# Optimization experiments

Measured on AMD Instinct MI355X. Metric: run time of the kernel, lower is better.

The kernel has to match this reference:

```python
import jax, jax.numpy as jnp
import numpy as np

B, N, D, EMB, H, W = 32, 20, 512, 512, 64, 64
TEMP = 10.0
EPS_IN = 1e-5


def setup_inputs() -> dict:
    key = jax.random.key(0)
    ks = jax.random.split(key, 12)
    fvisu = jax.random.normal(ks[0], (B, D, H, W), dtype=jnp.float32)
    fword = jax.random.normal(ks[1], (B, N, D), dtype=jnp.float32)
    context_score = jax.random.uniform(ks[2], (B, N), dtype=jnp.float32)
    # contiguous valid-token mask: lengths in [3, N-1] so CLS/SEP zeroing stays in range
    lengths = jax.random.randint(ks[3], (B,), 3, N)  # < N
    word_mask = (jnp.arange(N)[None, :] < lengths[:, None]).astype(jnp.int32)
    # params (kaiming-ish scale)
    def kinit(k, shape, fan_in):
        return jax.random.normal(k, shape, dtype=jnp.float32) * np.sqrt(2.0 / fan_in)
    attn_map_w = kinit(ks[4], (EMB // 2, D), D)          # Conv1d(512,256,1)
    attn_map_b = jnp.zeros((EMB // 2,), jnp.float32)
    attn_score_w = kinit(ks[5], (EMB // 2,), EMB // 2)   # Conv1d(256,1,1)
    attn_score_b = jnp.zeros((), jnp.float32)
    gamma_w = kinit(ks[6], (2 * EMB, D), D)              # Linear(512, 1024)
    gamma_b = jnp.zeros((2 * EMB,), jnp.float32)
    conv1_w = kinit(ks[7], (EMB, D), D)                  # Conv2d(512,512,1)
    conv1_b = jnp.zeros((EMB,), jnp.float32)
    return {
        "fvisu": fvisu, "fword": fword, "context_score": context_score,
        "attn_map_w": attn_map_w, "attn_map_b": attn_map_b,
        "attn_score_w": attn_score_w, "attn_score_b": attn_score_b,
        "gamma_w": gamma_w, "gamma_b": gamma_b,
        "conv1_w": conv1_w, "conv1_b": conv1_b,
        "word_mask": word_mask,
    }


def mask_softmax(attn_score, word_mask):
    # score = softmax(attn_score * T) over words
    score = jax.nn.softmax(attn_score * TEMP, axis=1)
    n = attn_score.shape[1]
    idx = jnp.arange(n)[None, :]
    m = word_mask[:, :n].astype(jnp.float32)
    m = m * (idx != 0)                                   # zero CLS
    s = m.sum(axis=1).astype(jnp.int32)                  # sum AFTER zeroing pos 0
    m = m * (idx != s[:, None])                          # zero SEP (last valid)
    ms = score * m
    return ms / (ms.sum(axis=1, keepdims=True) + 1e-8)


def reference(fvisu, fword, context_score, attn_map_w, attn_map_b,
              attn_score_w, attn_score_b, gamma_w, gamma_b,
              conv1_w, conv1_b, word_mask):
    # fword: [B,N,D] -> fw: [B,D,N]
    fw = jnp.transpose(fword, (0, 2, 1))
    # tile_visu: mean over spatial -> [B,D,1]
    tile_visu = jnp.mean(fvisu.reshape(fvisu.shape[0], fvisu.shape[1], -1), axis=2, keepdims=True)
    # prod fusion
    context_tile = tile_visu * fw * context_score[:, None, :]           # [B,D,N]
    attn_feat = jnp.tanh(jnp.einsum('oc,bcn->bon', attn_map_w, context_tile) + attn_map_b[None, :, None])
    attn_score = jnp.einsum('c,bcn->bn', attn_score_w, attn_feat) + attn_score_b  # [B,N]
    mask_score = mask_softmax(attn_score, word_mask)
    attn_lang_my = mask_score[:, None, :] * fw                          # [B,D,N]
    attn_lang = jnp.einsum('bn,bnd->bd', mask_score, fword)             # [B,D]
    # FiLM params
    film = attn_lang @ gamma_w.T + gamma_b                              # [B,2*EMB]
    gammas = jnp.tanh(film[:, :EMB])[:, :, None, None]
    betas = jnp.tanh(film[:, EMB:])[:, :, None, None]
    # conv1 (1x1) + InstanceNorm2d (no affine)
    fmodu = jnp.einsum('oc,bchw->bohw', conv1_w, fvisu) + conv1_b[None, :, None, None]
    mu = jnp.mean(fmodu, axis=(2, 3), keepdims=True)
    var = jnp.var(fmodu, axis=(2, 3), keepdims=True)
    fmodu = (fmodu - mu) * jax.lax.rsqrt(var + EPS_IN)
    fmodu = jax.nn.relu(gammas * fmodu + betas)
    return fmodu, attn_lang_my, attn_score
```

## Files before the change

kernel.cpp:

```cpp
#include <hip/hip_runtime.h>
#include <hip/hip_bf16.h>
#include <stdint.h>

#define NW 20
#define CD 512

typedef __attribute__((ext_vector_type(8))) short bhalf8;
typedef __attribute__((ext_vector_type(4))) float floatx4;

__device__ __forceinline__ uint16_t f2bf(float f){
    __hip_bfloat16 h = __float2bfloat16(f);
    return __builtin_bit_cast(uint16_t, h);
}
__device__ __forceinline__ float bf2f(uint16_t u){
    return __uint_as_float(((uint32_t)u) << 16);
}
__device__ __forceinline__ int hsw(int r){ return ((r >> 1) ^ (r >> 2)) & 7; }

__device__ __forceinline__ void gload16(const void* g, void* l){
    __builtin_amdgcn_global_load_lds(
        (const __attribute__((address_space(1))) uint32_t*)g,
        (__attribute__((address_space(3))) uint32_t*)l, 16, 0, 0);
}

__global__ void GroundTextBlock_context_49761491091856_kernel(int* p){ if (p) *p = 0; }

__global__ __launch_bounds__(256) void kprep(const float* __restrict__ w,
                                             uint16_t* __restrict__ warr){
    int ot = blockIdx.x >> 3, ks = blockIdx.x & 7;
    uint16_t* dst = warr + (size_t)blockIdx.x * 8192;
    for (int i = threadIdx.x; i < 8192; i += 256){
        int o = i >> 6, ke = i & 63;
        float v = w[(size_t)(ot * 128 + o) * 512 + ks * 64 + ke];
        int byteoff = o * 128 + ((((ke >> 3) ^ hsw(o)) << 4)) + ((ke & 7) << 1);
        dst[byteoff >> 1] = f2bf(v);
    }
}

__global__ __launch_bounds__(256) void kgemm(const float* __restrict__ fvisu,
                                             const uint16_t* __restrict__ warr,
                                             float* __restrict__ out0){
    __shared__ __align__(16) uint8_t Ab[16384];
    __shared__ __align__(16) uint8_t Bb[16384];
    __shared__ float tsum[CD];

    int lid = (int)((blockIdx.x & 7) * 512 + (blockIdx.x >> 3));
    int ot = lid & 3, jt = (lid >> 2) & 31, b = lid >> 7;

    int t = threadIdx.x;
    int lane = t & 63, wv = t >> 6;
    int wr = wv >> 1, wc = wv & 1;
    int l15 = lane & 15, l4 = lane >> 4;
    int cs0 = t >> 5, js = t & 31;
    int j0 = jt * 128;

    floatx4 acc[4][4];
    #pragma unroll
    for (int m = 0; m < 4; ++m)
        #pragma unroll
        for (int n = 0; n < 4; ++n)
            acc[m][n] = (floatx4){0.f, 0.f, 0.f, 0.f};

    for (int ks = 0; ks < 8; ++ks){
        if (ks) __syncthreads();
        {
            const uint8_t* asrc = (const uint8_t*)warr + (size_t)(ot * 8 + ks) * 16384;
            #pragma unroll
            for (int it = 0; it < 4; ++it){
                int lin = it * 4096 + t * 16;
                gload16(asrc + lin, Ab + lin);
            }
        }
        int k0 = ks * 64;
        #pragma unroll
        for (int blk = 0; blk < 2; ++blk){
            int cs = cs0 + blk * 8;
            float va[4][4];
            #pragma unroll
            for (int ci = 0; ci < 4; ++ci){
                const float* src = fvisu + (((size_t)(b * CD + k0 + cs * 4 + ci)) << 12) + j0 + js * 4;
                float4 v = *(const float4*)src;
                va[ci][0] = v.x; va[ci][1] = v.y; va[ci][2] = v.z; va[ci][3] = v.w;
            }
            if (ot == 0){
                #pragma unroll
                for (int ci = 0; ci < 4; ++ci){
                    float s = va[ci][0] + va[ci][1] + va[ci][2] + va[ci][3];
                    s += __shfl_xor(s, 1);  s += __shfl_xor(s, 2);
                    s += __shfl_xor(s, 4);  s += __shfl_xor(s, 8);
                    s += __shfl_xor(s, 16);
                    if ((lane & 31) == 0) tsum[k0 + cs * 4 + ci] = s;
                }
            }
            int unit = cs >> 1, half = cs & 1;
            #pragma unroll
            for (int jj = 0; jj < 4; ++jj){
                int j = js * 4 + jj;
                uint2 p;
                p.x = (uint32_t)f2bf(va[0][jj]) | ((uint32_t)f2bf(va[1][jj]) << 16);
                p.y = (uint32_t)f2bf(va[2][jj]) | ((uint32_t)f2bf(va[3][jj]) << 16);
                *(uint2*)(Bb + j * 128 + ((unit ^ hsw(j)) << 4) + half * 8) = p;
            }
        }
        __syncthreads();
        #pragma unroll
        for (int ksl = 0; ksl < 2; ++ksl){
            bhalf8 af[4], bfr[4];
            #pragma unroll
            for (int m = 0; m < 4; ++m){
                int o = wr * 64 + m * 16 + l15;
                int u = (ksl * 4 + l4) ^ hsw(o);
                af[m] = *(const bhalf8*)(Ab + o * 128 + (u << 4));
            }
            #pragma unroll
            for (int n = 0; n < 4; ++n){
                int j = wc * 64 + n * 16 + l15;
                int u = (ksl * 4 + l4) ^ hsw(j);
                bfr[n] = *(const bhalf8*)(Bb + j * 128 + (u << 4));
            }
            #pragma unroll
            for (int m = 0; m < 4; ++m)
                #pragma unroll
                for (int n = 0; n < 4; ++n)
                    acc[m][n] = __builtin_amdgcn_mfma_f32_16x16x32_bf16(af[m], bfr[n], acc[m][n], 0, 0, 0);
        }
    }
    if (ot == 0){
        __syncthreads();
        float* tp = out0 + (((size_t)(b * CD + jt)) << 12) + 2048;
        tp[t] = tsum[t];
        tp[t + 256] = tsum[t + 256];
    }
    uint16_t* sbase = (uint16_t*)out0;
    #pragma unroll
    for (int m = 0; m < 4; ++m){
        #pragma unroll
        for (int r = 0; r < 4; ++r){
            int o = ot * 128 + wr * 64 + m * 16 + l4 * 4 + r;
            uint16_t* row = sbase + ((size_t)(b * CD + o) << 13);
            #pragma unroll
            for (int n = 0; n < 4; ++n)
                row[j0 + wc * 64 + n * 16 + l15] = f2bf(acc[m][n][r]);
        }
    }
}

__global__ __launch_bounds__(256) void kattn(
    const float* __restrict__ fword, const float* __restrict__ cscore,
    const float* __restrict__ amw, const float* __restrict__ amb,
    const float* __restrict__ asw, const float* __restrict__ asb,
    const float* __restrict__ gw, const float* __restrict__ gb,
    const int* __restrict__ wmask, const float* __restrict__ out0,
    float* __restrict__ out1, float* __restrict__ out2,
    float* __restrict__ gam_arr, float* __restrict__ bet_arr)
{
    int b = blockIdx.x, t = threadIdx.x;
    __shared__ __align__(16) float fws[NW][CD];
    __shared__ __align__(16) float tl[CD];
    __shared__ __align__(16) float al[CD];
    __shared__ float css[NW];
    __shared__ int wm[NW];
    __shared__ float wred[4][NW];
    __shared__ float sc[NW];
    __shared__ float ms[NW];

    #pragma unroll
    for (int dd = 0; dd < 2; ++dd){
        int c = t + dd * 256;
        float s = 0.f;
        #pragma unroll 8
        for (int j2 = 0; j2 < 32; ++j2)
            s += out0[(((size_t)(b * CD + j2)) << 12) + 2048 + c];
        tl[c] = s * (1.f / 4096.f);
    }
    {
        const float4* src = (const float4*)(fword + (size_t)b * NW * CD);
        float4* dst = (float4*)&fws[0][0];
        for (int i = t; i < NW * CD / 4; i += 256) dst[i] = src[i];
    }
    if (t < NW){ css[t] = cscore[b * NW + t]; wm[t] = wmask[b * NW + t]; }
    __syncthreads();

    int o = t;
    float a[NW];
    #pragma unroll
    for (int n = 0; n < NW; ++n) a[n] = 0.f;
    {
        const float4* wrp = (const float4*)(amw + (size_t)o * CD);
        for (int c4 = 0; c4 < 128; ++c4){
            float4 wvv = wrp[c4];
            float4 tv = *(const float4*)(tl + c4 * 4);
            float wtx = wvv.x * tv.x, wty = wvv.y * tv.y, wtz = wvv.z * tv.z, wtw = wvv.w * tv.w;
            #pragma unroll
            for (int n = 0; n < NW; ++n){
                const float4 f = *(const float4*)(&fws[n][c4 * 4]);
                a[n] += wtx * f.x + wty * f.y + wtz * f.z + wtw * f.w;
            }
        }
    }
    {
        float aswo = asw[o], ambo = amb[o];
        #pragma unroll
        for (int n = 0; n < NW; ++n){
            float fo = aswo * tanhf(a[n] * css[n] + ambo);
            #pragma unroll
            for (int m = 1; m <= 32; m <<= 1) fo += __shfl_xor(fo, m);
            if ((t & 63) == 0) wred[t >> 6][n] = fo;
        }
    }
    __syncthreads();
    if (t < NW){
        float s = asb[0] + wred[0][t] + wred[1][t] + wred[2][t] + wred[3][t];
        sc[t] = s;
        out2[b * NW + t] = s;
    }
    __syncthreads();
    if (t < 64){
        float logit = (t < NW) ? sc[t] * 10.f : -1e30f;
        float mx = logit;
        #pragma unroll
        for (int m = 32; m >= 1; m >>= 1) mx = fmaxf(mx, __shfl_xor(mx, m));
        float e = (t < NW) ? expf(logit - mx) : 0.f;
        float den = e;
        #pragma unroll
        for (int m = 32; m >= 1; m >>= 1) den += __shfl_xor(den, m);
        float p = e / den;
        float m0 = (t > 0 && t < NW) ? (float)wm[t] : 0.f;
        float cnt = m0;
        #pragma unroll
        for (int m = 32; m >= 1; m >>= 1) cnt += __shfl_xor(cnt, m);
        int sidx = (int)(cnt + 0.5f);
        float m1 = (t == sidx) ? 0.f : m0;
        float msv = p * m1;
        float d2 = msv;
        #pragma unroll
        for (int m = 32; m >= 1; m >>= 1) d2 += __shfl_xor(d2, m);
        d2 += 1e-8f;
        if (t < NW) ms[t] = msv / d2;
    }
    __syncthreads();
    #pragma unroll
    for (int dd = 0; dd < 2; ++dd){
        int d = t + dd * 256;
        float acc_ = 0.f;
        float pk[NW];
        #pragma unroll
        for (int n = 0; n < NW; ++n){
            float v = ms[n] * fws[n][d];
            acc_ += v;
            pk[n] = v;
        }
        al[d] = acc_;
        float4* dst = (float4*)(out1 + (size_t)b * CD * NW + (size_t)d * NW);
        #pragma unroll
        for (int i = 0; i < NW / 4; ++i)
            dst[i] = make_float4(pk[i * 4], pk[i * 4 + 1], pk[i * 4 + 2], pk[i * 4 + 3]);
    }
    __syncthreads();
    #pragma unroll
    for (int kk = 0; kk < 4; ++kk){
        int k = kk * 256 + t;
        const float4* gr = (const float4*)(gw + (size_t)k * CD);
        float s = gb[k];
        for (int c4 = 0; c4 < 128; ++c4){
            float4 g4 = gr[c4];
            float4 a4 = *(const float4*)(al + c4 * 4);
            s += g4.x * a4.x + g4.y * a4.y + g4.z * a4.z + g4.w * a4.w;
        }
        float tv = tanhf(s);
        if (k < CD) gam_arr[b * CD + k] = tv;
        else        bet_arr[b * CD + (k - CD)] = tv;
    }
}

__global__ __launch_bounds__(256) void knormstat(
    float* __restrict__ out0, const float* __restrict__ gam_arr,
    const float* __restrict__ bet_arr)
{
    int bo = blockIdx.x, t = threadIdx.x;
    const uint16_t* srow = (const uint16_t*)out0 + ((size_t)bo << 13);
    float x[16];
    float s = 0.f, q = 0.f;
    #pragma unroll
    for (int h = 0; h < 2; ++h){
        uint4 v = *(const uint4*)(srow + (size_t)(h * 256 + t) * 8);
        uint32_t w[4] = {v.x, v.y, v.z, v.w};
        #pragma unroll
        for (int i = 0; i < 4; ++i){
            float x0 = bf2f((uint16_t)(w[i] & 0xffffu));
            float x1 = bf2f((uint16_t)(w[i] >> 16));
            x[h * 8 + i * 2]     = x0;
            x[h * 8 + i * 2 + 1] = x1;
            s += x0 + x1; q += x0 * x0 + x1 * x1;
        }
    }
    #pragma unroll
    for (int m = 1; m <= 32; m <<= 1){ s += __shfl_xor(s, m); q += __shfl_xor(q, m); }
    __shared__ float ss[4], qq[4];
    if ((t & 63) == 0){ ss[t >> 6] = s; qq[t >> 6] = q; }
    __syncthreads();
    float S = ss[0] + ss[1] + ss[2] + ss[3];
    float Q = qq[0] + qq[1] + qq[2] + qq[3];
    float mu = S * (1.f / 4096.f);
    float var = Q * (1.f / 4096.f) - mu * mu;
    float rs = rsqrtf(var + 1e-5f);
    float g = gam_arr[bo], be = bet_arr[bo];
    float4* drow = (float4*)(out0 + ((size_t)bo << 12));
    #pragma unroll
    for (int h = 0; h < 2; ++h){
        #pragma unroll
        for (int gix = 0; gix < 2; ++gix){
            float4 w4;
            w4.x = fmaxf(0.f, g * ((x[h * 8 + gix * 4 + 0] - mu) * rs) + be);
            w4.y = fmaxf(0.f, g * ((x[h * 8 + gix * 4 + 1] - mu) * rs) + be);
            w4.z = fmaxf(0.f, g * ((x[h * 8 + gix * 4 + 2] - mu) * rs) + be);
            w4.w = fmaxf(0.f, g * ((x[h * 8 + gix * 4 + 3] - mu) * rs) + be);
            drow[(size_t)(h * 256 + t) * 2 + gix] = w4;
        }
    }
}

extern "C" void kernel_launch(void* const* d_in, const int* in_sizes, int n_in,
                              void* d_out, int out_size, void* d_ws, size_t ws_size,
                              hipStream_t stream)
{
    const float* fvisu  = (const float*)d_in[0];
    const float* fword  = (const float*)d_in[1];
    const float* cscore = (const float*)d_in[2];
    const float* amw    = (const float*)d_in[3];
    const float* amb    = (const float*)d_in[4];
    const float* asw    = (const float*)d_in[5];
    const float* asb    = (const float*)d_in[6];
    const float* gw     = (const float*)d_in[7];
    const float* gb     = (const float*)d_in[8];
    const float* cw     = (const float*)d_in[9];
    const int* wmask    = (const int*)d_in[11];

    float* out0 = (float*)d_out;
    float* out1 = out0 + (size_t)67108864;
    float* out2 = out1 + (size_t)327680;

    uint8_t* ws = (uint8_t*)d_ws;
    uint16_t* warr = (uint16_t*)ws;
    float* gam_arr = (float*)(ws + 524288);
    float* bet_arr = (float*)(ws + 589824);

    kprep<<<32, 256, 0, stream>>>(cw, warr);
    kgemm<<<4096, 256, 0, stream>>>(fvisu, warr, out0);
    kattn<<<32, 256, 0, stream>>>(fword, cscore, amw, amb, asw, asb, gw, gb, wmask,
                                  out0, out1, out2, gam_arr, bet_arr);
    knormstat<<<16384, 256, 0, stream>>>(out0, gam_arr, bet_arr);
}
```

Baseline: 360.6 us.

## Double-buffer fvisu tile in LDS and read weight fragments directly from global

```diff
diff --git a/kernel.cpp b/kernel.cpp
--- a/kernel.cpp
+++ b/kernel.cpp
@@ -16,12 +16,6 @@
     return __uint_as_float(((uint32_t)u) << 16);
 }
 __device__ __forceinline__ int hsw(int r){ return ((r >> 1) ^ (r >> 2)) & 7; }
-
-__device__ __forceinline__ void gload16(const void* g, void* l){
-    __builtin_amdgcn_global_load_lds(
-        (const __attribute__((address_space(1))) uint32_t*)g,
-        (__attribute__((address_space(3))) uint32_t*)l, 16, 0, 0);
-}
 
 __global__ void GroundTextBlock_context_49761491091856_kernel(int* p){ if (p) *p = 0; }
 
@@ -40,8 +34,7 @@
 __global__ __launch_bounds__(256) void kgemm(const float* __restrict__ fvisu,
                                              const uint16_t* __restrict__ warr,
                                              float* __restrict__ out0){
-    __shared__ __align__(16) uint8_t Ab[16384];
-    __shared__ __align__(16) uint8_t Bb[16384];
+    __shared__ __align__(16) uint8_t Bb[2][16384];
     __shared__ float tsum[CD];
 
     int lid = (int)((blockIdx.x & 7) * 512 + (blockIdx.x >> 3));
@@ -61,48 +54,62 @@
         for (int n = 0; n < 4; ++n)
             acc[m][n] = (floatx4){0.f, 0.f, 0.f, 0.f};
 
+    const uint8_t* abase = (const uint8_t*)warr + (size_t)ot * 131072;
+    float va[2][4][4];
+
+    #pragma unroll
+    for (int blk = 0; blk < 2; ++blk){
+        int cs = cs0 + blk * 8;
+        #pragma unroll
+        for (int ci = 0; ci < 4; ++ci){
+            const float* src = fvisu + (((size_t)(b * CD + cs * 4 + ci)) << 12) + j0 + js * 4;
+            float4 v = *(const float4*)src;
+            va[blk][ci][0] = v.x; va[blk][ci][1] = v.y;
+            va[blk][ci][2] = v.z; va[blk][ci][3] = v.w;
+        }
+    }
+    #pragma unroll
+    for (int blk = 0; blk < 2; ++blk){
+        int cs = cs0 + blk * 8;
+        if (ot == 0){
+            #pragma unroll
+            for (int ci = 0; ci < 4; ++ci){
+                float s = va[blk][ci][0] + va[blk][ci][1] + va[blk][ci][2] + va[blk][ci][3];
+                s += __shfl_xor(s, 1);  s += __shfl_xor(s, 2);
+                s += __shfl_xor(s, 4);  s += __shfl_xor(s, 8);
+                s += __shfl_xor(s, 16);
+                if ((lane & 31) == 0) tsum[cs * 4 + ci] = s;
+            }
+        }
+        int unit = cs >> 1, half = cs & 1;
+        #pragma unroll
+        for (int jj = 0; jj < 4; ++jj){
+            int j = js * 4 + jj;
+            uint2 p;
+            p.x = (uint32_t)f2bf(va[blk][0][jj]) | ((uint32_t)f2bf(va[blk][1][jj]) << 16);
+            p.y = (uint32_t)f2bf(va[blk][2][jj]) | ((uint32_t)f2bf(va[blk][3][jj]) << 16);
+            *(uint2*)(Bb[0] + j * 128 + ((unit ^ hsw(j)) << 4) + half * 8) = p;
+        }
+    }
+    __syncthreads();
+
     for (int ks = 0; ks < 8; ++ks){
-        if (ks) __syncthreads();
-        {
-            const uint8_t* asrc = (const uint8_t*)warr + (size_t)(ot * 8 + ks) * 16384;
-            #pragma unroll
-            for (int it = 0; it < 4; ++it){
-                int lin = it * 4096 + t * 16;
-                gload16(asrc + lin, Ab + lin);
-            }
-        }
-        int k0 = ks * 64;
-        #pragma unroll
-        for (int blk = 0; blk < 2; ++blk){
-            int cs = cs0 + blk * 8;
-            float va[4][4];
-            #pragma unroll
-            for (int ci = 0; ci < 4; ++ci){
-                const float* src = fvisu + (((size_t)(b * CD + k0 + cs * 4 + ci)) << 12) + j0 + js * 4;
-                float4 v = *(const float4*)src;
-                va[ci][0] = v.x; va[ci][1] = v.y; va[ci][2] = v.z; va[ci][3] = v.w;
-            }
-            if (ot == 0){
+        int cur = ks & 1;
+        if (ks < 7){
+            int k1 = (ks + 1) * 64;
+            #pragma unroll
+            for (int blk = 0; blk < 2; ++blk){
+                int cs = cs0 + blk * 8;
                 #pragma unroll
                 for (int ci = 0; ci < 4; ++ci){
-                    float s = va[ci][0] + va[ci][1] + va[ci][2] + va[ci][3];
-                    s += __shfl_xor(s, 1);  s += __shfl_xor(s, 2);
-                    s += __shfl_xor(s, 4);  s += __shfl_xor(s, 8);
-                    s += __shfl_xor(s, 16);
-                    if ((lane & 31) == 0) tsum[k0 + cs * 4 + ci] = s;
+                    const float* src = fvisu + (((size_t)(b * CD + k1 + cs * 4 + ci)) << 12) + j0 + js * 4;
+                    float4 v = *(const float4*)src;
+                    va[blk][ci][0] = v.x; va[blk][ci][1] = v.y;
+                    va[blk][ci][2] = v.z; va[blk][ci][3] = v.w;
                 }
             }
-            int unit = cs >> 1, half = cs & 1;
-            #pragma unroll
-            for (int jj = 0; jj < 4; ++jj){
-                int j = js * 4 + jj;
-                uint2 p;
-                p.x = (uint32_t)f2bf(va[0][jj]) | ((uint32_t)f2bf(va[1][jj]) << 16);
-                p.y = (uint32_t)f2bf(va[2][jj]) | ((uint32_t)f2bf(va[3][jj]) << 16);
-                *(uint2*)(Bb + j * 128 + ((unit ^ hsw(j)) << 4) + half * 8) = p;
-            }
-        }
-        __syncthreads();
+        }
+        const uint8_t* atile = abase + (size_t)ks * 16384;
         #pragma unroll
         for (int ksl = 0; ksl < 2; ++ksl){
             bhalf8 af[4], bfr[4];
@@ -110,13 +117,13 @@
             for (int m = 0; m < 4; ++m){
                 int o = wr * 64 + m * 16 + l15;
                 int u = (ksl * 4 + l4) ^ hsw(o);
-                af[m] = *(const bhalf8*)(Ab + o * 128 + (u << 4));
+                af[m] = *(const bhalf8*)(atile + o * 128 + (u << 4));
             }
             #pragma unroll
             for (int n = 0; n < 4; ++n){
                 int j = wc * 64 + n * 16 + l15;
                 int u = (ksl * 4 + l4) ^ hsw(j);
-                bfr[n] = *(const bhalf8*)(Bb + j * 128 + (u << 4));
+                bfr[n] = *(const bhalf8*)(Bb[cur] + j * 128 + (u << 4));
             }
             #pragma unroll
             for (int m = 0; m < 4; ++m)
@@ -124,9 +131,36 @@
                 for (int n = 0; n < 4; ++n)
                     acc[m][n] = __builtin_amdgcn_mfma_f32_16x16x32_bf16(af[m], bfr[n], acc[m][n], 0, 0, 0);
         }
-    }
+        if (ks < 7){
+            int k1 = (ks + 1) * 64;
+            #pragma unroll
+            for (int blk = 0; blk < 2; ++blk){
+                int cs = cs0 + blk * 8;
+                if (ot == 0){
+                    #pragma unroll
+                    for (int ci = 0; ci < 4; ++ci){
+                        float s = va[blk][ci][0] + va[blk][ci][1] + va[blk][ci][2] + va[blk][ci][3];
+                        s += __shfl_xor(s, 1);  s += __shfl_xor(s, 2);
+                        s += __shfl_xor(s, 4);  s += __shfl_xor(s, 8);
+                        s += __shfl_xor(s, 16);
+                        if ((lane & 31) == 0) tsum[k1 + cs * 4 + ci] = s;
+                    }
+                }
+                int unit = cs >> 1, half = cs & 1;
+                #pragma unroll
+                for (int jj = 0; jj < 4; ++jj){
+                    int j = js * 4 + jj;
+                    uint2 p;
+                    p.x = (uint32_t)f2bf(va[blk][0][jj]) | ((uint32_t)f2bf(va[blk][1][jj]) << 16);
+                    p.y = (uint32_t)f2bf(va[blk][2][jj]) | ((uint32_t)f2bf(va[blk][3][jj]) << 16);
+                    *(uint2*)(Bb[cur ^ 1] + j * 128 + ((unit ^ hsw(j)) << 4) + half * 8) = p;
+                }
+            }
+        }
+        __syncthreads();
+    }
+
     if (ot == 0){
-        __syncthreads();
         float* tp = out0 + (((size_t)(b * CD + jt)) << 12) + 2048;
         tp[t] = tsum[t];
         tp[t + 256] = tsum[t + 256];
```

After: 402.2 us. 1.12x slower.
